# Performance work log

Measured on AMD Instinct MI355X. Metric: run time of the kernel, lower is better.

## Reference

```python
import jax, jax.numpy as jnp
import numpy as np
from jax import lax

WINDOW_SIZE = 11
SIGMA = 1.5
DATA_RANGE = 1.0
LEVELS = 4
EPS = 1e-8
DN = ('NCHW', 'OIHW', 'NCHW')


def _gauss1d(k, sigma):
    coords = jnp.arange(k, dtype=jnp.float32) - k // 2
    g = jnp.exp(-coords ** 2 / (2.0 * sigma ** 2))
    return g / g.sum()


def _blur(x, g):
    # separable depthwise Gaussian blur, VALID padding (use_padding=False)
    C = x.shape[1]
    k = g.shape[0]
    kw = jnp.broadcast_to(g.reshape(1, 1, 1, k), (C, 1, 1, k)).astype(x.dtype)
    kh = jnp.broadcast_to(g.reshape(1, 1, k, 1), (C, 1, k, 1)).astype(x.dtype)
    x = lax.conv_general_dilated(x, kw, (1, 1), 'VALID', dimension_numbers=DN, feature_group_count=C)
    x = lax.conv_general_dilated(x, kh, (1, 1), 'VALID', dimension_numbers=DN, feature_group_count=C)
    return x


def _avg_pool2(x):
    B, C, H, W = x.shape  # H, W even here (512 -> 64)
    return x.reshape(B, C, H // 2, 2, W // 2, 2).mean(axis=(3, 5))


def _ssim_level(X, Y, g):
    C1 = (0.01 * DATA_RANGE) ** 2
    C2 = (0.03 * DATA_RANGE) ** 2
    mu1 = _blur(X, g)
    mu2 = _blur(Y, g)
    sigma1_sq = _blur(X * X, g) - mu1 * mu1
    sigma2_sq = _blur(Y * Y, g) - mu2 * mu2
    sigma12 = _blur(X * Y, g) - mu1 * mu2
    cs_map = jax.nn.relu((2.0 * sigma12 + C2) / (sigma1_sq + sigma2_sq + C2))
    ssim_map = (2.0 * mu1 * mu2 + C1) / (mu1 * mu1 + mu2 * mu2 + C1) * cs_map
    return ssim_map.mean(axis=(1, 2, 3)), cs_map.mean(axis=(1, 2, 3))


def setup_inputs() -> dict:
    key = jax.random.key(0)
    kx, ky = jax.random.split(key)
    X = jax.random.uniform(kx, (16, 3, 512, 512), dtype=jnp.float32)
    Y = jax.random.uniform(ky, (16, 3, 512, 512), dtype=jnp.float32)
    return {'X': X, 'Y': Y}


def reference(X, Y):
    g = _gauss1d(WINDOW_SIZE, SIGMA)
    w = jnp.array([0.0448, 0.2856, 0.3001, 0.2363], dtype=jnp.float32)
    w = w / w.sum()
    vals = []
    for i in range(LEVELS):
        ss, cs = _ssim_level(X, Y, g)
        if i < LEVELS - 1:
            vals.append(cs)
            X = _avg_pool2(X)
            Y = _avg_pool2(Y)
        else:
            vals.append(ss)
    vals = jnp.maximum(jnp.stack(vals, axis=0), EPS)  # [levels, B]
    ms = jnp.prod(vals ** w[:, None], axis=0)
    return 1.0 - ms
```

## Files before the change

### kernel.cpp

```cpp
#include <hip/hip_runtime.h>
#include <math.h>

#define HALO 10
#define TS 32
#define IN 42
#define NP 22
#define XSTR 46
#define HSTR 46
#define NBIN 256

typedef float f2 __attribute__((ext_vector_type(2)));

struct GaussW { float g[11]; };

__global__ void init_acc_kernel(float* P) {
    int i = blockIdx.x * 256 + threadIdx.x;
    if (i < 4 * NBIN * 16) P[i] = 0.f;
}

__global__ __launch_bounds__(256, 4) void ssim_level_kernel(
    const float* __restrict__ X, const float* __restrict__ Y,
    int H, GaussW gw, float* __restrict__ Plevel, int last_level,
    float* __restrict__ Xpool, float* __restrict__ Ypool)
{
    const int W = H;
    const int Hout = H - HALO;

    __shared__ float Xs[IN][XSTR];
    __shared__ float Ys[IN][XSTR];
    __shared__ float Hs[4][TS][HSTR];
    __shared__ float red[4];

    const int tid = threadIdx.x;
    const int bc  = blockIdx.z;
    const int b   = bc / 3;
    const int r0  = blockIdx.y * TS;
    const int c0  = blockIdx.x * TS;
    const size_t base = (size_t)bc * H * W;

    for (int idx = tid; idx < IN * NP; idx += 256) {
        int rr = idx / NP, pp = idx - rr * NP;
        int gr = r0 + rr, gc = c0 + 2 * pp;
        float2 xv = make_float2(0.f, 0.f), yv = make_float2(0.f, 0.f);
        if (gr < H && gc < W) {
            const float* xp = X + base + (size_t)gr * W + gc;
            const float* yp = Y + base + (size_t)gr * W + gc;
            xv = *(const float2*)xp;
            yv = *(const float2*)yp;
        }
        *(float2*)&Xs[rr][2 * pp] = xv;
        *(float2*)&Ys[rr][2 * pp] = yv;
    }
    __syncthreads();

    if (tid < 168) {
        const int rr  = tid >> 2;
        const int seg = tid & 3;
        const int ccb = seg * 8;

        float x[20], y[20];
        #pragma unroll
        for (int u = 0; u < 10; ++u) {
            *(f2*)&x[2 * u] = *(const f2*)&Xs[rr][ccb + 2 * u];
            *(f2*)&y[2 * u] = *(const f2*)&Ys[rr][ccb + 2 * u];
        }

        #pragma unroll
        for (int p = 0; p < 4; ++p) {
            f2 ax = {0.f, 0.f}, ay = {0.f, 0.f};
            #pragma unroll
            for (int k = 0; k < 11; ++k) {
                f2 vx = { x[2 * p + k], x[2 * p + k + 1] };
                f2 vy = { y[2 * p + k], y[2 * p + k + 1] };
                ax += vx * gw.g[k];
                ay += vy * gw.g[k];
            }
            Hs[0][ccb + 2 * p    ][rr] = ax.x;
            Hs[0][ccb + 2 * p + 1][rr] = ax.y;
            Hs[1][ccb + 2 * p    ][rr] = ay.x;
            Hs[1][ccb + 2 * p + 1][rr] = ay.y;
        }
        #pragma unroll
        for (int i = 0; i < 9; ++i) {
            f2 xv = *(f2*)&x[2 * i];
            f2 yv = *(f2*)&y[2 * i];
            f2 a = xv + yv;
            f2 d = xv - yv;
            *(f2*)&x[2 * i] = a * a;
            *(f2*)&y[2 * i] = d * d;
        }
        #pragma unroll
        for (int p = 0; p < 4; ++p) {
            f2 as = {0.f, 0.f}, ad = {0.f, 0.f};
            #pragma unroll
            for (int k = 0; k < 11; ++k) {
                f2 vs = { x[2 * p + k], x[2 * p + k + 1] };
                f2 vd = { y[2 * p + k], y[2 * p + k + 1] };
                as += vs * gw.g[k];
                ad += vd * gw.g[k];
            }
            Hs[2][ccb + 2 * p    ][rr] = as.x;
            Hs[2][ccb + 2 * p + 1][rr] = as.y;
            Hs[3][ccb + 2 * p    ][rr] = ad.x;
            Hs[3][ccb + 2 * p + 1][rr] = ad.y;
        }
    } else if (tid >= 192 && !last_level) {
        const int t = tid - 192;
        const int Wp = W >> 1;
        #pragma unroll
        for (int q = 0; q < 4; ++q) {
            int cell = q * 64 + t;
            int pr = cell >> 4, pc = cell & 15;
            float2 xa = *(const float2*)&Xs[2 * pr][2 * pc];
            float2 xb = *(const float2*)&Xs[2 * pr + 1][2 * pc];
            float2 ya = *(const float2*)&Ys[2 * pr][2 * pc];
            float2 yb = *(const float2*)&Ys[2 * pr + 1][2 * pc];
            size_t o = (size_t)bc * (H >> 1) * Wp + (size_t)(r0 / 2 + pr) * Wp + (c0 / 2 + pc);
            Xpool[o] = 0.25f * (xa.x + xa.y + xb.x + xb.y);
            Ypool[o] = 0.25f * (ya.x + ya.y + yb.x + yb.y);
        }
    }
    __syncthreads();

    const int tx = tid & 31;
    const int ty = tid >> 5;
    const int rb = ty * 4;

    f2 m1[2], m2[2], S[2], D[2];
    #define VPASS(Q, OUT)                                                        \
    {                                                                            \
        float win[14];                                                           \
        _Pragma("unroll")                                                        \
        for (int i = 0; i < 7; ++i)                                              \
            *(f2*)&win[2 * i] = *(const f2*)&Hs[Q][tx][rb + 2 * i];              \
        _Pragma("unroll")                                                        \
        for (int h = 0; h < 2; ++h) {                                            \
            f2 acc = {0.f, 0.f};                                                 \
            _Pragma("unroll")                                                    \
            for (int k = 0; k < 11; ++k) {                                       \
                f2 v = { win[2 * h + k], win[2 * h + k + 1] };                   \
                acc += v * gw.g[k];                                              \
            }                                                                    \
            OUT[h] = acc;                                                        \
        }                                                                        \
    }
    VPASS(0, m1) VPASS(1, m2) VPASS(2, S) VPASS(3, D)
    #undef VPASS

    const float C1 = 1e-4f, C2 = 9e-4f;
    float acc_s = 0.f;
    #pragma unroll
    for (int o = 0; o < 4; ++o) {
        float u1 = m1[o >> 1][o & 1], u2 = m2[o >> 1][o & 1];
        float Sv = S[o >> 1][o & 1],  Dv = D[o >> 1][o & 1];
        float u1s = u1 * u1, u2s = u2 * u2, u12 = u1 * u2;
        float ssum = 0.5f  * (Sv + Dv);
        float sxy  = 0.25f * (Sv - Dv);
        float vsum = ssum - u1s - u2s;
        float v12  = sxy - u12;
        float A2   = fmaxf(2.f * v12 + C2, 0.f);
        float B1   = u1s + u2s + C1;
        float B2   = vsum + C2;
        float inv  = __builtin_amdgcn_rcpf(B1 * B2);
        float val;
        if (!last_level) {
            val = A2 * B1 * inv;
        } else {
            float A1 = 2.f * u12 + C1;
            val = A1 * A2 * inv;
        }
        bool valid = (r0 + rb + o < Hout) && (c0 + tx < Hout);
        acc_s += valid ? val : 0.f;
    }

    #pragma unroll
    for (int off = 32; off; off >>= 1) acc_s += __shfl_down(acc_s, off);
    if ((tid & 63) == 0) red[tid >> 6] = acc_s;
    __syncthreads();
    if (tid == 0) {
        int lin = blockIdx.x + gridDim.x * (blockIdx.y + gridDim.y * blockIdx.z);
        int bin = lin & (NBIN - 1);
        atomicAdd(&Plevel[bin * 16 + b], red[0] + red[1] + red[2] + red[3]);
    }
}

__global__ void finalize_kernel(const float* __restrict__ P, float* __restrict__ out) {
    __shared__ float red[64][4];
    const int tid  = threadIdx.x;
    const int pair = tid >> 2;
    const int chnk = tid & 3;
    const int l = pair >> 4, b = pair & 15;
    float s = 0.f;
    #pragma unroll 4
    for (int j = 0; j < 64; ++j)
        s += P[((l * NBIN) + (chnk * 64) + j) * 16 + b];
    red[pair][chnk] = s;
    __syncthreads();
    if (tid < 16) {
        const int bb = tid;
        const float wraw[4] = {0.0448f, 0.2856f, 0.3001f, 0.2363f};
        float wsum = wraw[0] + wraw[1] + wraw[2] + wraw[3];
        float ms = 1.f;
        for (int ll = 0; ll < 4; ++ll) {
            int Hh = 512 >> ll;
            int Ho = Hh - HALO;
            float cnt = 3.f * (float)Ho * (float)Ho;
            float val = (red[ll * 16 + bb][0] + red[ll * 16 + bb][1] +
                         red[ll * 16 + bb][2] + red[ll * 16 + bb][3]) / cnt;
            val = fmaxf(val, 1e-8f);
            ms *= powf(val, wraw[ll] / wsum);
        }
        out[bb] = 1.f - ms;
    }
}

extern "C" void kernel_launch(void* const* d_in, const int* in_sizes, int n_in,
                              void* d_out, int out_size, void* d_ws, size_t ws_size,
                              hipStream_t stream)
{
    const float* X0 = (const float*)d_in[0];
    const float* Y0 = (const float*)d_in[1];
    float* out = (float*)d_out;
    float* ws  = (float*)d_ws;

    const size_t PSZ = (size_t)4 * NBIN * 16;
    float* P  = ws;
    float* X1 = ws + PSZ;
    float* Y1 = X1 + (size_t)16 * 3 * 256 * 256;
    float* X2 = Y1 + (size_t)16 * 3 * 256 * 256;
    float* Y2 = X2 + (size_t)16 * 3 * 128 * 128;
    float* X3 = Y2 + (size_t)16 * 3 * 128 * 128;
    float* Y3 = X3 + (size_t)16 * 3 * 64 * 64;

    GaussW gw;
    {
        float s = 0.f;
        for (int i = 0; i < 11; ++i) {
            float d = (float)(i - 5);
            gw.g[i] = expf(-d * d / (2.f * 1.5f * 1.5f));
            s += gw.g[i];
        }
        for (int i = 0; i < 11; ++i) gw.g[i] /= s;
    }

    hipLaunchKernelGGL(init_acc_kernel, dim3((4 * NBIN * 16 + 255) / 256), dim3(256), 0, stream, P);

    hipLaunchKernelGGL(ssim_level_kernel, dim3(16, 16, 48), dim3(256), 0, stream,
                       X0, Y0, 512, gw, P + 0 * NBIN * 16, 0, X1, Y1);
    hipLaunchKernelGGL(ssim_level_kernel, dim3(8, 8, 48),   dim3(256), 0, stream,
                       X1, Y1, 256, gw, P + 1 * NBIN * 16, 0, X2, Y2);
    hipLaunchKernelGGL(ssim_level_kernel, dim3(4, 4, 48),   dim3(256), 0, stream,
                       X2, Y2, 128, gw, P + 2 * NBIN * 16, 0, X3, Y3);
    hipLaunchKernelGGL(ssim_level_kernel, dim3(2, 2, 48),   dim3(256), 0, stream,
                       X3, Y3, 64,  gw, P + 3 * NBIN * 16, 1, (float*)nullptr, (float*)nullptr);

    hipLaunchKernelGGL(finalize_kernel, dim3(1), dim3(256), 0, stream, P, out);
}
```

Baseline: 206.8 us.

## Fuse all pyramid levels into one persistent cooperative kernel with grid syncs

Replaces six separate launches (init, four per-level SSIM kernels, finalize) with a single cooperative persistent kernel. Blocks loop over tiles per level, with grid.sync between levels and the finalize step in block 0. This removes launch gaps and tail idle time between the small later levels. In exchange it adds grid-wide barrier cost and caps occupancy at a fixed resident grid, which the large level-0 tile loop now has to cover.

```diff
diff --git a/kernel.cpp b/kernel.cpp
--- a/kernel.cpp
+++ b/kernel.cpp
@@ -1,5 +1,8 @@
 #include <hip/hip_runtime.h>
+#include <hip/hip_cooperative_groups.h>
 #include <math.h>
+
+namespace cg = cooperative_groups;
 
 #define HALO 10
 #define TS 32
@@ -13,29 +16,28 @@
 
 struct GaussW { float g[11]; };
 
-__global__ void init_acc_kernel(float* P) {
-    int i = blockIdx.x * 256 + threadIdx.x;
-    if (i < 4 * NBIN * 16) P[i] = 0.f;
-}
-
-__global__ __launch_bounds__(256, 4) void ssim_level_kernel(
+__device__ void process_tile(
     const float* __restrict__ X, const float* __restrict__ Y,
-    int H, GaussW gw, float* __restrict__ Plevel, int last_level,
-    float* __restrict__ Xpool, float* __restrict__ Ypool)
+    int H, int l2x, const GaussW& gw, float* __restrict__ Plevel, int last_level,
+    float* __restrict__ Xpool, float* __restrict__ Ypool, int t)
 {
-    const int W = H;
-    const int Hout = H - HALO;
-
     __shared__ float Xs[IN][XSTR];
     __shared__ float Ys[IN][XSTR];
     __shared__ float Hs[4][TS][HSTR];
     __shared__ float red[4];
 
+    const int W = H;
+    const int Hout = H - HALO;
+
     const int tid = threadIdx.x;
-    const int bc  = blockIdx.z;
+    const int ntx   = 1 << l2x;
+    const int bc  = t >> (2 * l2x);
+    const int rem = t & (ntx * ntx - 1);
+    const int by  = rem >> l2x;
+    const int bx  = rem & (ntx - 1);
     const int b   = bc / 3;
-    const int r0  = blockIdx.y * TS;
-    const int c0  = blockIdx.x * TS;
+    const int r0  = by * TS;
+    const int c0  = bx * TS;
     const size_t base = (size_t)bc * H * W;
 
     for (int idx = tid; idx < IN * NP; idx += 256) {
@@ -105,11 +107,11 @@
             Hs[3][ccb + 2 * p + 1][rr] = ad.y;
         }
     } else if (tid >= 192 && !last_level) {
-        const int t = tid - 192;
+        const int tt = tid - 192;
         const int Wp = W >> 1;
         #pragma unroll
         for (int q = 0; q < 4; ++q) {
-            int cell = q * 64 + t;
+            int cell = q * 64 + tt;
             int pr = cell >> 4, pc = cell & 15;
             float2 xa = *(const float2*)&Xs[2 * pr][2 * pc];
             float2 xb = *(const float2*)&Xs[2 * pr + 1][2 * pc];
@@ -178,39 +180,73 @@
     if ((tid & 63) == 0) red[tid >> 6] = acc_s;
     __syncthreads();
     if (tid == 0) {
-        int lin = blockIdx.x + gridDim.x * (blockIdx.y + gridDim.y * blockIdx.z);
-        int bin = lin & (NBIN - 1);
+        int bin = t & (NBIN - 1);
         atomicAdd(&Plevel[bin * 16 + b], red[0] + red[1] + red[2] + red[3]);
     }
+    __syncthreads();
 }
 
-__global__ void finalize_kernel(const float* __restrict__ P, float* __restrict__ out) {
-    __shared__ float red[64][4];
-    const int tid  = threadIdx.x;
-    const int pair = tid >> 2;
-    const int chnk = tid & 3;
-    const int l = pair >> 4, b = pair & 15;
-    float s = 0.f;
-    #pragma unroll 4
-    for (int j = 0; j < 64; ++j)
-        s += P[((l * NBIN) + (chnk * 64) + j) * 16 + b];
-    red[pair][chnk] = s;
-    __syncthreads();
-    if (tid < 16) {
-        const int bb = tid;
-        const float wraw[4] = {0.0448f, 0.2856f, 0.3001f, 0.2363f};
-        float wsum = wraw[0] + wraw[1] + wraw[2] + wraw[3];
-        float ms = 1.f;
-        for (int ll = 0; ll < 4; ++ll) {
-            int Hh = 512 >> ll;
-            int Ho = Hh - HALO;
-            float cnt = 3.f * (float)Ho * (float)Ho;
-            float val = (red[ll * 16 + bb][0] + red[ll * 16 + bb][1] +
-                         red[ll * 16 + bb][2] + red[ll * 16 + bb][3]) / cnt;
-            val = fmaxf(val, 1e-8f);
-            ms *= powf(val, wraw[ll] / wsum);
-        }
-        out[bb] = 1.f - ms;
+__global__ __launch_bounds__(256, 4) void msssim_mega(
+    const float* __restrict__ X0, const float* __restrict__ Y0,
+    float* __restrict__ P,
+    float* __restrict__ X1, float* __restrict__ Y1,
+    float* __restrict__ X2, float* __restrict__ Y2,
+    float* __restrict__ X3, float* __restrict__ Y3,
+    GaussW gw, float* __restrict__ out)
+{
+    cg::grid_group grid = cg::this_grid();
+    const int tid = threadIdx.x;
+
+    {
+        int idx = blockIdx.x * 256 + tid;
+        if (idx < 4 * NBIN * 16) P[idx] = 0.f;
+    }
+    __threadfence();
+    grid.sync();
+
+    const float* Xl[4] = {X0, X1, X2, X3};
+    const float* Yl[4] = {Y0, Y1, Y2, Y3};
+    float* Xp[4] = {X1, X2, X3, nullptr};
+    float* Yp[4] = {Y1, Y2, Y3, nullptr};
+    const int Hl[4]     = {512, 256, 128, 64};
+    const int l2xl[4]   = {4, 3, 2, 1};
+    const int ntile[4]  = {12288, 3072, 768, 192};
+
+    for (int l = 0; l < 4; ++l) {
+        for (int t = blockIdx.x; t < ntile[l]; t += gridDim.x)
+            process_tile(Xl[l], Yl[l], Hl[l], l2xl[l], gw, P + l * NBIN * 16,
+                         l == 3, Xp[l], Yp[l], t);
+        __threadfence();
+        grid.sync();
+    }
+
+    if (blockIdx.x == 0) {
+        __shared__ float fred[64][4];
+        const int pair = tid >> 2;
+        const int chnk = tid & 3;
+        const int l = pair >> 4, b = pair & 15;
+        float s = 0.f;
+        #pragma unroll 4
+        for (int j = 0; j < 64; ++j)
+            s += P[((l * NBIN) + (chnk * 64) + j) * 16 + b];
+        fred[pair][chnk] = s;
+        __syncthreads();
+        if (tid < 16) {
+            const int bb = tid;
+            const float wraw[4] = {0.0448f, 0.2856f, 0.3001f, 0.2363f};
+            float wsum = wraw[0] + wraw[1] + wraw[2] + wraw[3];
+            float ms = 1.f;
+            for (int ll = 0; ll < 4; ++ll) {
+                int Hh = 512 >> ll;
+                int Ho = Hh - HALO;
+                float cnt = 3.f * (float)Ho * (float)Ho;
+                float val = (fred[ll * 16 + bb][0] + fred[ll * 16 + bb][1] +
+                             fred[ll * 16 + bb][2] + fred[ll * 16 + bb][3]) / cnt;
+                val = fmaxf(val, 1e-8f);
+                ms *= powf(val, wraw[ll] / wsum);
+            }
+            out[bb] = 1.f - ms;
+        }
     }
 }
 
@@ -243,16 +279,16 @@
         for (int i = 0; i < 11; ++i) gw.g[i] /= s;
     }
 
-    hipLaunchKernelGGL(init_acc_kernel, dim3((4 * NBIN * 16 + 255) / 256), dim3(256), 0, stream, P);
-
-    hipLaunchKernelGGL(ssim_level_kernel, dim3(16, 16, 48), dim3(256), 0, stream,
-                       X0, Y0, 512, gw, P + 0 * NBIN * 16, 0, X1, Y1);
-    hipLaunchKernelGGL(ssim_level_kernel, dim3(8, 8, 48),   dim3(256), 0, stream,
-                       X1, Y1, 256, gw, P + 1 * NBIN * 16, 0, X2, Y2);
-    hipLaunchKernelGGL(ssim_level_kernel, dim3(4, 4, 48),   dim3(256), 0, stream,
-                       X2, Y2, 128, gw, P + 2 * NBIN * 16, 0, X3, Y3);
-    hipLaunchKernelGGL(ssim_level_kernel, dim3(2, 2, 48),   dim3(256), 0, stream,
-                       X3, Y3, 64,  gw, P + 3 * NBIN * 16, 1, (float*)nullptr, (float*)nullptr);
-
-    hipLaunchKernelGGL(finalize_kernel, dim3(1), dim3(256), 0, stream, P, out);
+    int maxB = 0;
+    hipOccupancyMaxActiveBlocksPerMultiprocessor(&maxB, msssim_mega, 256, 0);
+    if (maxB < 1) maxB = 1;
+    if (maxB > 4) maxB = 4;
+    int grid = maxB * 256;
+
+    void* args[] = {
+        (void*)&X0, (void*)&Y0, (void*)&P,
+        (void*)&X1, (void*)&Y1, (void*)&X2, (void*)&Y2, (void*)&X3, (void*)&Y3,
+        (void*)&gw, (void*)&out
+    };
+    hipLaunchCooperativeKernel((void*)msssim_mega, dim3(grid), dim3(256), args, 0, stream);
 }
```

Result: slower. 703.3 us (+240.1%).

## Load inputs directly to registers, drop input LDS tiles and atomics

Applied to the files above, without the earlier changes.

Drops the shared-memory staging of the X/Y input tile: each horizontal-pass thread reads its 20-element row segment from global memory with float4 loads, and the pooling threads read global memory directly. The vertical pass moves to 128 threads each computing 8 rows, and per-block partial sums go to fixed slots instead of binned atomics, which removes the init kernel. The smaller LDS footprint allows launch bounds of 5 blocks per SM. In exchange, overlapping halo reads across threads rely on the cache, and half the threads sit idle during the vertical pass.

```diff
diff --git a/kernel.cpp b/kernel.cpp
--- a/kernel.cpp
+++ b/kernel.cpp
@@ -4,65 +4,63 @@
 #define HALO 10
 #define TS 32
 #define IN 42
-#define NP 22
-#define XSTR 46
 #define HSTR 46
-#define NBIN 256
 
 typedef float f2 __attribute__((ext_vector_type(2)));
 
 struct GaussW { float g[11]; };
 
-__global__ void init_acc_kernel(float* P) {
-    int i = blockIdx.x * 256 + threadIdx.x;
-    if (i < 4 * NBIN * 16) P[i] = 0.f;
-}
-
-__global__ __launch_bounds__(256, 4) void ssim_level_kernel(
+#define P2_TOTAL 16320
+
+__global__ __launch_bounds__(256, 5) void ssim_level_kernel(
     const float* __restrict__ X, const float* __restrict__ Y,
-    int H, GaussW gw, float* __restrict__ Plevel, int last_level,
+    int H, GaussW gw, float* __restrict__ P2lvl, int last_level,
     float* __restrict__ Xpool, float* __restrict__ Ypool)
 {
     const int W = H;
     const int Hout = H - HALO;
 
-    __shared__ float Xs[IN][XSTR];
-    __shared__ float Ys[IN][XSTR];
     __shared__ float Hs[4][TS][HSTR];
     __shared__ float red[4];
 
     const int tid = threadIdx.x;
     const int bc  = blockIdx.z;
-    const int b   = bc / 3;
     const int r0  = blockIdx.y * TS;
     const int c0  = blockIdx.x * TS;
     const size_t base = (size_t)bc * H * W;
-
-    for (int idx = tid; idx < IN * NP; idx += 256) {
-        int rr = idx / NP, pp = idx - rr * NP;
-        int gr = r0 + rr, gc = c0 + 2 * pp;
-        float2 xv = make_float2(0.f, 0.f), yv = make_float2(0.f, 0.f);
-        if (gr < H && gc < W) {
-            const float* xp = X + base + (size_t)gr * W + gc;
-            const float* yp = Y + base + (size_t)gr * W + gc;
-            xv = *(const float2*)xp;
-            yv = *(const float2*)yp;
-        }
-        *(float2*)&Xs[rr][2 * pp] = xv;
-        *(float2*)&Ys[rr][2 * pp] = yv;
-    }
-    __syncthreads();
 
     if (tid < 168) {
         const int rr  = tid >> 2;
         const int seg = tid & 3;
         const int ccb = seg * 8;
+        const int gr  = r0 + rr;
+        const int gc0 = c0 + ccb;
+        const bool rowok = (gr < H);
 
         float x[20], y[20];
-        #pragma unroll
-        for (int u = 0; u < 10; ++u) {
-            *(f2*)&x[2 * u] = *(const f2*)&Xs[rr][ccb + 2 * u];
-            *(f2*)&y[2 * u] = *(const f2*)&Ys[rr][ccb + 2 * u];
+        if (rowok && (gc0 + 20 <= W)) {
+            const float* xp = X + base + (size_t)gr * W + gc0;
+            const float* yp = Y + base + (size_t)gr * W + gc0;
+            #pragma unroll
+            for (int v = 0; v < 5; ++v) {
+                float4 xv = *(const float4*)(xp + 4 * v);
+                float4 yv = *(const float4*)(yp + 4 * v);
+                x[4*v+0] = xv.x; x[4*v+1] = xv.y; x[4*v+2] = xv.z; x[4*v+3] = xv.w;
+                y[4*v+0] = yv.x; y[4*v+1] = yv.y; y[4*v+2] = yv.z; y[4*v+3] = yv.w;
+            }
+        } else {
+            const int grc = rowok ? gr : (H - 1);
+            const float* xp = X + base + (size_t)grc * W;
+            const float* yp = Y + base + (size_t)grc * W;
+            #pragma unroll
+            for (int i = 0; i < 20; ++i) {
+                int gc  = gc0 + i;
+                int gcc = gc < W ? gc : (W - 1);
+                bool ok = rowok && (gc < W);
+                float xv = xp[gcc], yv = yp[gcc];
+                x[i] = ok ? xv : 0.f;
+                y[i] = ok ? yv : 0.f;
+            }
         }
 
         #pragma unroll
@@ -111,10 +109,11 @@
         for (int q = 0; q < 4; ++q) {
             int cell = q * 64 + t;
             int pr = cell >> 4, pc = cell & 15;
-            float2 xa = *(const float2*)&Xs[2 * pr][2 * pc];
-            float2 xb = *(const float2*)&Xs[2 * pr + 1][2 * pc];
-            float2 ya = *(const float2*)&Ys[2 * pr][2 * pc];
-            float2 yb = *(const float2*)&Ys[2 * pr + 1][2 * pc];
+            const size_t srow = base + (size_t)(r0 + 2 * pr) * W + (c0 + 2 * pc);
+            float2 xa = *(const float2*)(X + srow);
+            float2 xb = *(const float2*)(X + srow + W);
+            float2 ya = *(const float2*)(Y + srow);
+            float2 yb = *(const float2*)(Y + srow + W);
             size_t o = (size_t)bc * (H >> 1) * Wp + (size_t)(r0 / 2 + pr) * Wp + (c0 / 2 + pc);
             Xpool[o] = 0.25f * (xa.x + xa.y + xb.x + xb.y);
             Ypool[o] = 0.25f * (ya.x + ya.y + yb.x + yb.y);
@@ -122,55 +121,57 @@
     }
     __syncthreads();
 
-    const int tx = tid & 31;
-    const int ty = tid >> 5;
-    const int rb = ty * 4;
-
-    f2 m1[2], m2[2], S[2], D[2];
-    #define VPASS(Q, OUT)                                                        \
-    {                                                                            \
-        float win[14];                                                           \
-        _Pragma("unroll")                                                        \
-        for (int i = 0; i < 7; ++i)                                              \
-            *(f2*)&win[2 * i] = *(const f2*)&Hs[Q][tx][rb + 2 * i];              \
-        _Pragma("unroll")                                                        \
-        for (int h = 0; h < 2; ++h) {                                            \
-            f2 acc = {0.f, 0.f};                                                 \
+    float acc_s = 0.f;
+    if (tid < 128) {
+        const int tx = tid & 31;
+        const int tg = tid >> 5;
+        const int rb = tg * 8;
+
+        f2 m1[4], m2[4], S[4], D[4];
+        #define VPASS(Q, OUT)                                                    \
+        {                                                                        \
+            float win[18];                                                       \
             _Pragma("unroll")                                                    \
-            for (int k = 0; k < 11; ++k) {                                       \
-                f2 v = { win[2 * h + k], win[2 * h + k + 1] };                   \
-                acc += v * gw.g[k];                                              \
+            for (int i = 0; i < 9; ++i)                                          \
+                *(f2*)&win[2 * i] = *(const f2*)&Hs[Q][tx][rb + 2 * i];          \
+            _Pragma("unroll")                                                    \
+            for (int h = 0; h < 4; ++h) {                                        \
+                f2 a = {0.f, 0.f};                                               \
+                _Pragma("unroll")                                                \
+                for (int k = 0; k < 11; ++k) {                                   \
+                    f2 v = { win[2 * h + k], win[2 * h + k + 1] };               \
+                    a += v * gw.g[k];                                            \
+                }                                                                \
+                OUT[h] = a;                                                      \
             }                                                                    \
-            OUT[h] = acc;                                                        \
-        }                                                                        \
-    }
-    VPASS(0, m1) VPASS(1, m2) VPASS(2, S) VPASS(3, D)
-    #undef VPASS
-
-    const float C1 = 1e-4f, C2 = 9e-4f;
-    float acc_s = 0.f;
-    #pragma unroll
-    for (int o = 0; o < 4; ++o) {
-        float u1 = m1[o >> 1][o & 1], u2 = m2[o >> 1][o & 1];
-        float Sv = S[o >> 1][o & 1],  Dv = D[o >> 1][o & 1];
-        float u1s = u1 * u1, u2s = u2 * u2, u12 = u1 * u2;
-        float ssum = 0.5f  * (Sv + Dv);
-        float sxy  = 0.25f * (Sv - Dv);
-        float vsum = ssum - u1s - u2s;
-        float v12  = sxy - u12;
-        float A2   = fmaxf(2.f * v12 + C2, 0.f);
-        float B1   = u1s + u2s + C1;
-        float B2   = vsum + C2;
-        float inv  = __builtin_amdgcn_rcpf(B1 * B2);
-        float val;
-        if (!last_level) {
-            val = A2 * B1 * inv;
-        } else {
-            float A1 = 2.f * u12 + C1;
-            val = A1 * A2 * inv;
-        }
-        bool valid = (r0 + rb + o < Hout) && (c0 + tx < Hout);
-        acc_s += valid ? val : 0.f;
+        }
+        VPASS(0, m1) VPASS(1, m2) VPASS(2, S) VPASS(3, D)
+        #undef VPASS
+
+        const float C1 = 1e-4f, C2 = 9e-4f;
+        #pragma unroll
+        for (int o = 0; o < 8; ++o) {
+            float u1 = m1[o >> 1][o & 1], u2 = m2[o >> 1][o & 1];
+            float Sv = S[o >> 1][o & 1],  Dv = D[o >> 1][o & 1];
+            float u1s = u1 * u1, u2s = u2 * u2, u12 = u1 * u2;
+            float ssum = 0.5f  * (Sv + Dv);
+            float sxy  = 0.25f * (Sv - Dv);
+            float vsum = ssum - u1s - u2s;
+            float v12  = sxy - u12;
+            float A2   = fmaxf(2.f * v12 + C2, 0.f);
+            float B1   = u1s + u2s + C1;
+            float B2   = vsum + C2;
+            float inv  = __builtin_amdgcn_rcpf(B1 * B2);
+            float val;
+            if (!last_level) {
+                val = A2 * B1 * inv;
+            } else {
+                float A1 = 2.f * u12 + C1;
+                val = A1 * A2 * inv;
+            }
+            bool valid = (r0 + rb + o < Hout) && (c0 + tx < Hout);
+            acc_s += valid ? val : 0.f;
+        }
     }
 
     #pragma unroll
@@ -179,21 +180,22 @@
     __syncthreads();
     if (tid == 0) {
         int lin = blockIdx.x + gridDim.x * (blockIdx.y + gridDim.y * blockIdx.z);
-        int bin = lin & (NBIN - 1);
-        atomicAdd(&Plevel[bin * 16 + b], red[0] + red[1] + red[2] + red[3]);
+        P2lvl[lin] = red[0] + red[1];
     }
 }
 
-__global__ void finalize_kernel(const float* __restrict__ P, float* __restrict__ out) {
+__global__ void finalize_kernel(const float* __restrict__ P2, float* __restrict__ out) {
     __shared__ float red[64][4];
     const int tid  = threadIdx.x;
     const int pair = tid >> 2;
     const int chnk = tid & 3;
     const int l = pair >> 4, b = pair & 15;
+    const int off[4]  = {0, 12288, 15360, 16128};
+    const int nper[4] = {768, 192, 48, 12};
+    const int n4 = nper[l] >> 2;
+    const float* p = P2 + off[l] + b * nper[l] + chnk * n4;
     float s = 0.f;
-    #pragma unroll 4
-    for (int j = 0; j < 64; ++j)
-        s += P[((l * NBIN) + (chnk * 64) + j) * 16 + b];
+    for (int j = 0; j < n4; ++j) s += p[j];
     red[pair][chnk] = s;
     __syncthreads();
     if (tid < 16) {
@@ -223,9 +225,8 @@
     float* out = (float*)d_out;
     float* ws  = (float*)d_ws;
 
-    const size_t PSZ = (size_t)4 * NBIN * 16;
-    float* P  = ws;
-    float* X1 = ws + PSZ;
+    float* P2 = ws;
+    float* X1 = ws + P2_TOTAL;
     float* Y1 = X1 + (size_t)16 * 3 * 256 * 256;
     float* X2 = Y1 + (size_t)16 * 3 * 256 * 256;
     float* Y2 = X2 + (size_t)16 * 3 * 128 * 128;
@@ -243,16 +244,14 @@
         for (int i = 0; i < 11; ++i) gw.g[i] /= s;
     }
 
-    hipLaunchKernelGGL(init_acc_kernel, dim3((4 * NBIN * 16 + 255) / 256), dim3(256), 0, stream, P);
-
     hipLaunchKernelGGL(ssim_level_kernel, dim3(16, 16, 48), dim3(256), 0, stream,
-                       X0, Y0, 512, gw, P + 0 * NBIN * 16, 0, X1, Y1);
+                       X0, Y0, 512, gw, P2 + 0,     0, X1, Y1);
     hipLaunchKernelGGL(ssim_level_kernel, dim3(8, 8, 48),   dim3(256), 0, stream,
-                       X1, Y1, 256, gw, P + 1 * NBIN * 16, 0, X2, Y2);
+                       X1, Y1, 256, gw, P2 + 12288, 0, X2, Y2);
     hipLaunchKernelGGL(ssim_level_kernel, dim3(4, 4, 48),   dim3(256), 0, stream,
-                       X2, Y2, 128, gw, P + 2 * NBIN * 16, 0, X3, Y3);
+                       X2, Y2, 128, gw, P2 + 15360, 0, X3, Y3);
     hipLaunchKernelGGL(ssim_level_kernel, dim3(2, 2, 48),   dim3(256), 0, stream,
-                       X3, Y3, 64,  gw, P + 3 * NBIN * 16, 1, (float*)nullptr, (float*)nullptr);
-
-    hipLaunchKernelGGL(finalize_kernel, dim3(1), dim3(256), 0, stream, P, out);
+                       X3, Y3, 64,  gw, P2 + 16128, 1, (float*)nullptr, (float*)nullptr);
+
+    hipLaunchKernelGGL(finalize_kernel, dim3(1), dim3(256), 0, stream, P2, out);
 }
```

New measurement: 240.9 us. 1.17x slower.
